# Optimization experiments

Hardware: AMD Instinct MI355X
Metric: run time of the kernel (lower is better)

Reference implementation:

```python
import jax, jax.numpy as jnp
import numpy as np

KS = 5
SIGMA = 2.0
N_BINS = 50
MOMENTUM = 0.9
HALF_KS = (KS - 1) // 2


def _gaussian_kernel_window(ks=KS, sigma=SIGMA):
    # Replicates scipy.ndimage.gaussian_filter1d(delta, sigma, mode='reflect'),
    # then renormalizes, exactly as FDS._get_kernel_window does.
    half = (ks - 1) // 2
    base = np.zeros(ks, np.float32)
    base[half] = 1.0
    r = int(4.0 * sigma + 0.5)  # scipy default truncate=4.0
    j = np.arange(-r, r + 1)
    w = np.exp(-0.5 * (j / sigma) ** 2)
    w = w / w.sum()
    idx = np.arange(-r, ks + r)
    for _ in range(8):  # repeated 'reflect' (edge-excluding-center style: d c b a | a b c d | d c b a)
        idx = np.where(idx < 0, -idx - 1, idx)
        idx = np.where(idx >= ks, 2 * ks - 1 - idx, idx)
    xp = base[idx]
    out = np.array([float(np.dot(w, xp[i:i + 2 * r + 1])) for i in range(ks)], np.float32)
    return out / out.sum()


def setup_inputs() -> dict:
    key = jax.random.key(0)
    k1, k2, k3, k4 = jax.random.split(key, 4)
    N, D = 262144, 512
    features = jax.random.normal(k1, (N, D), dtype=jnp.float32)
    labels = jax.random.randint(k2, (N,), 0, N_BINS, dtype=jnp.int64)
    running_mean = jax.random.normal(k3, (N_BINS, D), dtype=jnp.float32)
    running_var = jax.random.uniform(k4, (N_BINS, D), dtype=jnp.float32) + 0.5
    num_samples_tracked = jnp.zeros((N_BINS,), dtype=jnp.float32)
    kernel_window = jnp.asarray(_gaussian_kernel_window(), dtype=jnp.float32)
    return {
        "features": features,
        "labels": labels,
        "running_mean": running_mean,
        "running_var": running_var,
        "num_samples_tracked": num_samples_tracked,
        "kernel_window": kernel_window,
    }


def _smooth(x, kernel_window):
    # reflect-pad (torch 'reflect': excludes edge) along bin axis, then cross-correlate (F.conv1d)
    top = x[HALF_KS:0:-1]              # [half_ks, D]
    bot = x[-2:-2 - HALF_KS:-1]        # [half_ks, D]
    xp = jnp.concatenate([top, x, bot], axis=0)  # [B + 2*half_ks, D]
    B = x.shape[0]
    windows = jnp.stack([xp[i:i + B] for i in range(KS)], axis=0)  # [ks, B, D]
    return jnp.einsum("k,kbd->bd", kernel_window, windows)


def reference(features, labels, running_mean, running_var, num_samples_tracked, kernel_window):
    # --- segmented per-bin mean/var (single pass, replaces the Python loop over labels) ---
    N = features.shape[0]
    labels = labels.astype(jnp.int32)
    counts = jax.ops.segment_sum(jnp.ones((N,), features.dtype), labels, num_segments=N_BINS)  # [B]
    sums = jax.ops.segment_sum(features, labels, num_segments=N_BINS)                          # [B, D]
    sumsq = jax.ops.segment_sum(features * features, labels, num_segments=N_BINS)              # [B, D]
    safe_n = jnp.maximum(counts, 1.0)
    mean = sums / safe_n[:, None]
    # unbiased var for n>1; biased (=0) for n==1, matching torch.var unbiased toggle
    var = (sumsq - safe_n[:, None] * mean * mean) / jnp.maximum(counts - 1.0, 1.0)[:, None]

    present = (counts > 0)[:, None]
    f = MOMENTUM
    new_mean = jnp.where(present, (1.0 - f) * mean + f * running_mean, running_mean)
    new_var = jnp.where(present, (1.0 - f) * var + f * running_var, running_var)
    new_num = num_samples_tracked + counts

    # --- update_smoothed_stats: conv1d smoothing over the bin axis ---
    smoothed_mean = _smooth(new_mean, kernel_window)
    smoothed_var = _smooth(new_var, kernel_window)
    return new_mean, new_var, new_num, smoothed_mean, smoothed_var
```

## Files before the change

kernel.cpp:

```cpp
#include <hip/hip_runtime.h>

#define NB 50
#define DD 512
#define KSZ 5
#define SORT_ROWS 4096
#define EPT 16
#define RPW 512
#define COLG 8
#define UNR 8

__global__ __launch_bounds__(256) void fds_sort(
    const int* __restrict__ labels,
    int*       __restrict__ packed,
    float*     __restrict__ g_cnt)
{
    __shared__ int s_hist[NB];
    __shared__ int s_cur[NB];
    const int tid  = threadIdx.x;
    const int base = blockIdx.x * SORT_ROWS;

    if (tid < NB) s_hist[tid] = 0;
    __syncthreads();

    int lab[EPT];
#pragma unroll
    for (int j = 0; j < EPT; ++j) {
        lab[j] = labels[base + j * 256 + tid];
        __hip_atomic_fetch_add(&s_hist[lab[j]], 1,
                               __ATOMIC_RELAXED, __HIP_MEMORY_SCOPE_WORKGROUP);
    }
    __syncthreads();

    if (tid == 0) {
        int run = 0;
        for (int b = 0; b < NB; ++b) { s_cur[b] = run; run += s_hist[b]; }
    }
    __syncthreads();

    if (tid < NB)
        __hip_atomic_fetch_add(&g_cnt[tid], (float)s_hist[tid],
                               __ATOMIC_RELAXED, __HIP_MEMORY_SCOPE_AGENT);

#pragma unroll
    for (int j = 0; j < EPT; ++j) {
        const int l   = lab[j];
        const int pos = __hip_atomic_fetch_add(&s_cur[l], 1,
                              __ATOMIC_RELAXED, __HIP_MEMORY_SCOPE_WORKGROUP);
        const int row = base + j * 256 + tid;
        packed[base + pos] = (row << 6) | l;
    }
}

__global__ __launch_bounds__(256) void fds_reduce(
    const float* __restrict__ features,
    const int*   __restrict__ packed,
    float* __restrict__ g_sum,
    float* __restrict__ g_sq)
{
    const int tid  = threadIdx.x;
    const int wave = tid >> 6;
    const int lane = tid & 63;
    const int gw   = blockIdx.x * 4 + wave;
    const int cg     = gw & (COLG - 1);
    const int rchunk = gw >> 3;
    const int col = cg * 64 + lane;
    const int r0  = rchunk * RPW;

    float sum = 0.f, sq = 0.f;
    int cur = packed[r0] & 63;

    int pk[UNR];
#pragma unroll
    for (int j = 0; j < UNR; ++j) pk[j] = packed[r0 + j];

    for (int it = 0; it < RPW; it += UNR) {
        float v[UNR];
#pragma unroll
        for (int j = 0; j < UNR; ++j)
            v[j] = features[(size_t)(pk[j] >> 6) * DD + col];

        int pk2[UNR];
        const int nb = (it + UNR < RPW) ? (r0 + it + UNR) : r0;
#pragma unroll
        for (int j = 0; j < UNR; ++j) pk2[j] = packed[nb + j];

#pragma unroll
        for (int j = 0; j < UNR; ++j) {
            const int l = pk[j] & 63;
            if (l != cur) {
                __hip_atomic_fetch_add(&g_sum[cur * DD + col], sum,
                                       __ATOMIC_RELAXED, __HIP_MEMORY_SCOPE_AGENT);
                __hip_atomic_fetch_add(&g_sq [cur * DD + col], sq,
                                       __ATOMIC_RELAXED, __HIP_MEMORY_SCOPE_AGENT);
                sum = 0.f; sq = 0.f; cur = l;
            }
            sum += v[j];
            sq = fmaf(v[j], v[j], sq);
        }
#pragma unroll
        for (int j = 0; j < UNR; ++j) pk[j] = pk2[j];
    }
    __hip_atomic_fetch_add(&g_sum[cur * DD + col], sum,
                           __ATOMIC_RELAXED, __HIP_MEMORY_SCOPE_AGENT);
    __hip_atomic_fetch_add(&g_sq [cur * DD + col], sq,
                           __ATOMIC_RELAXED, __HIP_MEMORY_SCOPE_AGENT);
}

__global__ __launch_bounds__(256) void fds_finalize(
    const float* __restrict__ g_sum, const float* __restrict__ g_sq,
    const float* __restrict__ g_cnt,
    const float* __restrict__ running_mean, const float* __restrict__ running_var,
    const float* __restrict__ num_tracked, const float* __restrict__ kwin,
    float* __restrict__ out)
{
    __shared__ float s_cnt[NB];
    __shared__ float s_w[KSZ];
    const int tid = threadIdx.x;
    if (tid < NB)  s_cnt[tid] = g_cnt[tid];
    if (tid < KSZ) s_w[tid]   = kwin[tid];
    __syncthreads();

    const int idx = blockIdx.x * 256 + tid;
    const int b = idx / DD;
    const int d = idx - b * DD;

    float sm = 0.f, sv = 0.f, my_nm = 0.f, my_nv = 0.f;
#pragma unroll
    for (int k = 0; k < KSZ; ++k) {
        const int i = b + k;
        const int bb = (i < 2) ? (2 - i) : ((i >= NB + 2) ? (2 * NB - i) : (i - 2));
        const float cnt    = s_cnt[bb];
        const float safe_n = fmaxf(cnt, 1.f);
        const float s   = g_sum[bb * DD + d];
        const float sqv = g_sq [bb * DD + d];
        const float mean = s / safe_n;
        const float var  = (sqv - safe_n * mean * mean) / fmaxf(cnt - 1.f, 1.f);
        const float rm = running_mean[bb * DD + d];
        const float rv = running_var [bb * DD + d];
        float nm, nv;
        if (cnt > 0.f) {
            nm = 0.1f * mean + 0.9f * rm;
            nv = 0.1f * var  + 0.9f * rv;
        } else {
            nm = rm; nv = rv;
        }
        sm += s_w[k] * nm;
        sv += s_w[k] * nv;
        if (k == 2) { my_nm = nm; my_nv = nv; }
    }
    out[idx]                    = my_nm;
    out[NB * DD + idx]          = my_nv;
    out[2 * NB * DD + NB + idx] = sm;
    out[3 * NB * DD + NB + idx] = sv;
    if (idx < NB)
        out[2 * NB * DD + idx] = num_tracked[idx] + s_cnt[idx];
}

extern "C" void kernel_launch(void* const* d_in, const int* in_sizes, int n_in,
                              void* d_out, int out_size, void* d_ws, size_t ws_size,
                              hipStream_t stream)
{
    const float* features     = (const float*)d_in[0];
    const int*   labels       = (const int*)  d_in[1];
    const float* running_mean = (const float*)d_in[2];
    const float* running_var  = (const float*)d_in[3];
    const float* num_tracked  = (const float*)d_in[4];
    const float* kwin         = (const float*)d_in[5];
    float* out = (float*)d_out;

    const int N = in_sizes[1];

    float* g_sum  = (float*)d_ws;
    float* g_sq   = g_sum + NB * DD;
    float* g_cnt  = g_sq  + NB * DD;
    int*   packed = (int*)(g_cnt + NB);

    hipMemsetAsync(d_ws, 0, (size_t)(2 * NB * DD + NB) * sizeof(float), stream);

    fds_sort<<<N / SORT_ROWS, 256, 0, stream>>>(labels, packed, g_cnt);

    fds_reduce<<<(N / RPW) * COLG / 4, 256, 0, stream>>>(features, packed, g_sum, g_sq);

    fds_finalize<<<NB * DD / 256, 256, 0, stream>>>(
        g_sum, g_sq, g_cnt, running_mean, running_var, num_tracked, kwin, out);
}
```

Baseline: 707.9 us.

## Give each wave full rows with float4 loads and scalar row indices

The reduce kernel now has each wave cover a whole 512-wide feature row, each lane loading two float4 chunks, instead of splitting columns into 8 groups of 64 floats. Row chunks shrink from 512 to 64 rows per wave, and packed indices are read with readfirstlane so they stay in scalar registers. The aim is wider, fully coalesced 2 KB row loads and fewer redundant reads of the packed index stream. In exchange, each segment flush now issues 16 atomics per lane and the smaller chunks mean more flushes overall.

```diff
diff --git a/kernel.cpp b/kernel.cpp
--- a/kernel.cpp
+++ b/kernel.cpp
@@ -5,8 +5,7 @@
 #define KSZ 5
 #define SORT_ROWS 4096
 #define EPT 16
-#define RPW 512
-#define COLG 8
+#define RPC 64
 #define UNR 8
 
 __global__ __launch_bounds__(256) void fds_sort(
@@ -60,50 +59,74 @@
     const int tid  = threadIdx.x;
     const int wave = tid >> 6;
     const int lane = tid & 63;
-    const int gw   = blockIdx.x * 4 + wave;
-    const int cg     = gw & (COLG - 1);
-    const int rchunk = gw >> 3;
-    const int col = cg * 64 + lane;
-    const int r0  = rchunk * RPW;
-
-    float sum = 0.f, sq = 0.f;
-    int cur = packed[r0] & 63;
+    const int chunk = blockIdx.x * 4 + wave;
+    const int r0 = chunk * RPC;
+    const int c0 = lane * 4;
+
+    float4 s0 = {0,0,0,0}, s1 = {0,0,0,0};
+    float4 q0 = {0,0,0,0}, q1 = {0,0,0,0};
 
     int pk[UNR];
 #pragma unroll
-    for (int j = 0; j < UNR; ++j) pk[j] = packed[r0 + j];
-
-    for (int it = 0; it < RPW; it += UNR) {
-        float v[UNR];
+    for (int j = 0; j < UNR; ++j)
+        pk[j] = __builtin_amdgcn_readfirstlane(packed[r0 + j]);
+    int cur = pk[0] & 63;
+
+    for (int it = 0; it < RPC; it += UNR) {
+        float4 v0[UNR], v1[UNR];
+#pragma unroll
+        for (int j = 0; j < UNR; ++j) {
+            const float* rp = features + (size_t)(pk[j] >> 6) * DD;
+            v0[j] = *(const float4*)(rp + c0);
+            v1[j] = *(const float4*)(rp + 256 + c0);
+        }
+
+        int pk2[UNR];
+        const int nb = (it + UNR < RPC) ? (r0 + it + UNR) : r0;
 #pragma unroll
         for (int j = 0; j < UNR; ++j)
-            v[j] = features[(size_t)(pk[j] >> 6) * DD + col];
-
-        int pk2[UNR];
-        const int nb = (it + UNR < RPW) ? (r0 + it + UNR) : r0;
-#pragma unroll
-        for (int j = 0; j < UNR; ++j) pk2[j] = packed[nb + j];
+            pk2[j] = __builtin_amdgcn_readfirstlane(packed[nb + j]);
 
 #pragma unroll
         for (int j = 0; j < UNR; ++j) {
             const int l = pk[j] & 63;
             if (l != cur) {
-                __hip_atomic_fetch_add(&g_sum[cur * DD + col], sum,
-                                       __ATOMIC_RELAXED, __HIP_MEMORY_SCOPE_AGENT);
-                __hip_atomic_fetch_add(&g_sq [cur * DD + col], sq,
-                                       __ATOMIC_RELAXED, __HIP_MEMORY_SCOPE_AGENT);
-                sum = 0.f; sq = 0.f; cur = l;
+                float* ps = &g_sum[cur * DD + c0];
+                float* pq = &g_sq [cur * DD + c0];
+#pragma unroll
+                for (int k = 0; k < 4; ++k) {
+                    __hip_atomic_fetch_add(ps + k,       (&s0.x)[k], __ATOMIC_RELAXED, __HIP_MEMORY_SCOPE_AGENT);
+                    __hip_atomic_fetch_add(ps + 256 + k, (&s1.x)[k], __ATOMIC_RELAXED, __HIP_MEMORY_SCOPE_AGENT);
+                    __hip_atomic_fetch_add(pq + k,       (&q0.x)[k], __ATOMIC_RELAXED, __HIP_MEMORY_SCOPE_AGENT);
+                    __hip_atomic_fetch_add(pq + 256 + k, (&q1.x)[k], __ATOMIC_RELAXED, __HIP_MEMORY_SCOPE_AGENT);
+                }
+                s0 = {0,0,0,0}; s1 = {0,0,0,0};
+                q0 = {0,0,0,0}; q1 = {0,0,0,0};
+                cur = l;
             }
-            sum += v[j];
-            sq = fmaf(v[j], v[j], sq);
+#pragma unroll
+            for (int k = 0; k < 4; ++k) {
+                (&s0.x)[k] += (&v0[j].x)[k];
+                (&q0.x)[k] = fmaf((&v0[j].x)[k], (&v0[j].x)[k], (&q0.x)[k]);
+                (&s1.x)[k] += (&v1[j].x)[k];
+                (&q1.x)[k] = fmaf((&v1[j].x)[k], (&v1[j].x)[k], (&q1.x)[k]);
+            }
         }
 #pragma unroll
         for (int j = 0; j < UNR; ++j) pk[j] = pk2[j];
     }
-    __hip_atomic_fetch_add(&g_sum[cur * DD + col], sum,
-                           __ATOMIC_RELAXED, __HIP_MEMORY_SCOPE_AGENT);
-    __hip_atomic_fetch_add(&g_sq [cur * DD + col], sq,
-                           __ATOMIC_RELAXED, __HIP_MEMORY_SCOPE_AGENT);
+
+    {
+        float* ps = &g_sum[cur * DD + c0];
+        float* pq = &g_sq [cur * DD + c0];
+#pragma unroll
+        for (int k = 0; k < 4; ++k) {
+            __hip_atomic_fetch_add(ps + k,       (&s0.x)[k], __ATOMIC_RELAXED, __HIP_MEMORY_SCOPE_AGENT);
+            __hip_atomic_fetch_add(ps + 256 + k, (&s1.x)[k], __ATOMIC_RELAXED, __HIP_MEMORY_SCOPE_AGENT);
+            __hip_atomic_fetch_add(pq + k,       (&q0.x)[k], __ATOMIC_RELAXED, __HIP_MEMORY_SCOPE_AGENT);
+            __hip_atomic_fetch_add(pq + 256 + k, (&q1.x)[k], __ATOMIC_RELAXED, __HIP_MEMORY_SCOPE_AGENT);
+        }
+    }
 }
 
 __global__ __launch_bounds__(256) void fds_finalize(
@@ -179,7 +202,7 @@
 
     fds_sort<<<N / SORT_ROWS, 256, 0, stream>>>(labels, packed, g_cnt);
 
-    fds_reduce<<<(N / RPW) * COLG / 4, 256, 0, stream>>>(features, packed, g_sum, g_sq);
+    fds_reduce<<<N / RPC / 4, 256, 0, stream>>>(features, packed, g_sum, g_sq);
 
     fds_finalize<<<NB * DD / 256, 256, 0, stream>>>(
         g_sum, g_sq, g_cnt, running_mean, running_var, num_tracked, kwin, out);
```

Result: slower. 724.2 us (+2.3%).
